# Kernel optimization log

Measured on AMD Instinct MI355X. Metric: run time of the kernel, lower is better.

## Reference

```python
import jax, jax.numpy as jnp
import numpy as np

N = 10000
F_IN = 512
HID = 256
C = 16
N_POST_ITER = 4


def setup_inputs() -> dict:
    key = jax.random.key(0)
    ks = jax.random.split(key, 10)
    raw_adj = jax.random.uniform(ks[0], (N, N), dtype=jnp.float32) * 0.01
    A = jax.random.uniform(ks[1], (N, N), dtype=jnp.float32)
    normed_adj = A / jnp.sum(A, axis=1, keepdims=True)  # row-sum-one normalized
    features = jax.random.normal(ks[2], (N, F_IN), dtype=jnp.float32)
    labels = jax.random.randint(ks[3], (N,), 0, C)
    y_onehot = jax.nn.one_hot(labels, C, dtype=jnp.float32)
    train_mask = jax.random.randint(ks[4], (N,), 0, 2).astype(jnp.bool_)
    # GCN belief estimator params (glorot-ish scaling)
    W1 = jax.random.normal(ks[5], (F_IN, HID), dtype=jnp.float32) / np.sqrt(F_IN)
    b1 = jnp.zeros((HID,), dtype=jnp.float32)
    W2 = jax.random.normal(ks[6], (HID, C), dtype=jnp.float32) / np.sqrt(HID)
    b2 = jnp.zeros((C,), dtype=jnp.float32)
    # class-compatibility matrix H (initialized, zero-centered as in init_H)
    H = jax.random.normal(ks[7], (C, C), dtype=jnp.float32) * 0.1
    return {"raw_adj": raw_adj, "normed_adj": normed_adj, "features": features,
            "y_onehot": y_onehot, "train_mask": train_mask,
            "W1": W1, "b1": b1, "W2": W2, "b2": b2, "H": H}


def reference(raw_adj, normed_adj, features, y_onehot, train_mask, W1, b1, W2, b2, H):
    num_class = y_onehot.shape[1]
    # 2-layer GCN belief estimator: adj @ (x @ W) + b
    h = jax.nn.relu(normed_adj @ (features @ W1) + b1)          # [N, HID]
    logits = normed_adj @ (h @ W2) + b2                          # [N, C]
    # post_process: iterative compatibility-guided belief propagation
    prior_belief = jax.nn.softmax(logits, axis=1)
    E_hat = prior_belief - 1.0 / num_class
    B_hat = E_hat
    for _ in range(N_POST_ITER):
        B_hat = E_hat + raw_adj @ (B_hat @ H)
    post_belief = B_hat + 1.0 / num_class
    return post_belief
```

## Files before the change

kernel.cpp:

```cpp
#include <hip/hip_runtime.h>

#define NN 10000
#define KP 10048
static constexpr float INV_C = 1.0f / 16.0f;

typedef __attribute__((ext_vector_type(8))) short bf16x8;
typedef __attribute__((ext_vector_type(4))) float f32x4;
typedef unsigned short u16;
typedef unsigned int u32;

__device__ __forceinline__ u16 f2b(float f) {
    union { float f; u32 u; } v; v.f = f;
    u32 r = v.u + 0x7FFFu + ((v.u >> 16) & 1u);
    return (u16)(r >> 16);
}

#define AS1(p) ((__attribute__((address_space(1))) void*)(p))
#define AS3(p) ((__attribute__((address_space(3))) void*)(p))

__global__ __launch_bounds__(256)
void cvt_feat(const float* __restrict__ src, u16* __restrict__ dst)
{
    int c = blockIdx.x * 256 + threadIdx.x;
    size_t base = (size_t)c * 8;
    const float4* s4 = (const float4*)(src + base);
    float4 a = s4[0], b = s4[1];
    bf16x8 o;
    o[0]=f2b(a.x); o[1]=f2b(a.y); o[2]=f2b(a.z); o[3]=f2b(a.w);
    o[4]=f2b(b.x); o[5]=f2b(b.y); o[6]=f2b(b.z); o[7]=f2b(b.w);
    *(bf16x8*)(dst + base) = o;
}

__global__ __launch_bounds__(256)
void w12t(const float* __restrict__ W1, const float* __restrict__ W2,
          float* __restrict__ W1T, u16* __restrict__ W2T)
{
    int bid = blockIdx.x, t = threadIdx.x;
    if (bid < 512) {
        int idx = bid * 256 + t;
        int n = idx >> 9, k = idx & 511;
        W1T[idx] = W1[(size_t)k * 256 + n];
    } else {
        int idx = (bid - 512) * 256 + t;
        if (idx < 4096) {
            int n_ = idx >> 8, k_ = idx & 255;
            W2T[idx] = f2b(W2[(size_t)k_ * 16 + n_]);
        }
    }
}

template<int BIAS, int RELU>
__global__ __launch_bounds__(256)
void gemm_a32_bt16(const float* __restrict__ A, int lda, int M, int Ka,
                   const u16* __restrict__ BT, int ldb, int N, int npad,
                   const float* __restrict__ bias,
                   u16* __restrict__ C, int ldc, int K)
{
    __shared__ u16 Asm[64 * 64];
    __shared__ u16 Bsm[256 * 64];
    const int t = threadIdx.x;
    const int lane = t & 63;
    const int w = t >> 6;
    const int row0 = blockIdx.x * 64;
    const int n0 = blockIdx.y * 256;

    const f32x4 fz = {0.f, 0.f, 0.f, 0.f};
    f32x4 acc[4][4];
#pragma unroll
    for (int i = 0; i < 4; ++i)
#pragma unroll
        for (int j = 0; j < 4; ++j) acc[i][j] = fz;

    const int ar = t >> 2, akq = t & 3;
    int agr = row0 + ar; if (agr > M - 1) agr = M - 1;
    const float* asrc = A + (size_t)agr * lda + akq * 16;
    const int aslot0 = (akq * 2) ^ (ar & 7);
    const int aslot1 = (akq * 2 + 1) ^ (ar & 7);
    const int l8 = lane >> 3, sl = lane & 7;

    for (int k0 = 0; k0 < K; k0 += 64) {
#pragma unroll
        for (int i = 0; i < 8; ++i) {
            int lr = i * 32 + w * 8 + l8;
            int gn = n0 + lr; if (gn > N - 1) gn = N - 1;
            int ss = sl ^ (lr & 7);
            const u16* src = BT + (size_t)gn * ldb + k0 + ss * 8;
            __builtin_amdgcn_global_load_lds(AS1(src), AS3(&Bsm[(i * 32 + w * 8) * 64]),
                                             16, 0, 0);
        }
        bool aval = (k0 + akq * 16) < Ka;
        float4 x0, x1, x2, x3;
        if (aval) {
            x0 = *(const float4*)(asrc + k0);
            x1 = *(const float4*)(asrc + k0 + 4);
            x2 = *(const float4*)(asrc + k0 + 8);
            x3 = *(const float4*)(asrc + k0 + 12);
        } else {
            x0 = x1 = x2 = x3 = make_float4(0.f, 0.f, 0.f, 0.f);
        }
        bf16x8 p0, p1;
        p0[0]=f2b(x0.x); p0[1]=f2b(x0.y); p0[2]=f2b(x0.z); p0[3]=f2b(x0.w);
        p0[4]=f2b(x1.x); p0[5]=f2b(x1.y); p0[6]=f2b(x1.z); p0[7]=f2b(x1.w);
        p1[0]=f2b(x2.x); p1[1]=f2b(x2.y); p1[2]=f2b(x2.z); p1[3]=f2b(x2.w);
        p1[4]=f2b(x3.x); p1[5]=f2b(x3.y); p1[6]=f2b(x3.z); p1[7]=f2b(x3.w);
        *(bf16x8*)&Asm[ar * 64 + aslot0 * 8] = p0;
        *(bf16x8*)&Asm[ar * 64 + aslot1 * 8] = p1;
        __syncthreads();
#pragma unroll
        for (int kk = 0; kk < 2; ++kk) {
            bf16x8 afr[4], bfr[4];
#pragma unroll
            for (int mi = 0; mi < 4; ++mi) {
                int r = mi * 16 + (lane & 15);
                int s2 = (kk * 4 + (lane >> 4)) ^ (r & 7);
                afr[mi] = *(const bf16x8*)&Asm[r * 64 + s2 * 8];
            }
#pragma unroll
            for (int ni = 0; ni < 4; ++ni) {
                int nr = w * 64 + ni * 16 + (lane & 15);
                int s2 = (kk * 4 + (lane >> 4)) ^ (nr & 7);
                bfr[ni] = *(const bf16x8*)&Bsm[nr * 64 + s2 * 8];
            }
#pragma unroll
            for (int mi = 0; mi < 4; ++mi)
#pragma unroll
                for (int ni = 0; ni < 4; ++ni)
                    acc[mi][ni] = __builtin_amdgcn_mfma_f32_16x16x32_bf16(
                        afr[mi], bfr[ni], acc[mi][ni], 0, 0, 0);
        }
        __syncthreads();
    }
#pragma unroll
    for (int mi = 0; mi < 4; ++mi) {
        int grb = row0 + mi * 16 + (lane >> 4) * 4;
#pragma unroll
        for (int ni = 0; ni < 4; ++ni) {
            int gc = n0 + w * 64 + ni * 16 + (lane & 15);
            if (gc < npad) {
                float bv = (BIAS && gc < N) ? bias[gc] : 0.f;
#pragma unroll
                for (int rg = 0; rg < 4; ++rg) {
                    int gr = grb + rg;
                    if (gr < M) {
                        float v = acc[mi][ni][rg] + bv;
                        if (RELU) v = fmaxf(v, 0.f);
                        C[(size_t)gr * ldc + gc] = f2b(gc < N ? v : 0.f);
                    }
                }
            }
        }
    }
}

template<int CVT>
__global__ __launch_bounds__(256)
void gemm_na(const float* __restrict__ A, const u16* __restrict__ BT,
             float* __restrict__ Pws, u16* __restrict__ Acvt)
{
    __shared__ u16 Asm[64 * 64];
    __shared__ u16 Bsm[256 * 64];
    const int t = threadIdx.x;
    const int lane = t & 63;
    const int w = t >> 6;
    const int row0 = blockIdx.x * 64;
    const int s = blockIdx.y;
    const int c0 = (157 * s) >> 3, c1 = (157 * (s + 1)) >> 3;

    const f32x4 fz = {0.f, 0.f, 0.f, 0.f};
    f32x4 acc[4][4];
#pragma unroll
    for (int i = 0; i < 4; ++i)
#pragma unroll
        for (int j = 0; j < 4; ++j) acc[i][j] = fz;

    const int ar = t >> 2, akq = t & 3;
    const int grow = row0 + ar;
    const int agr = grow < NN ? grow : NN - 1;
    const float* asrc = A + (size_t)agr * NN + akq * 16;
    const int aslot0 = (akq * 2) ^ (ar & 7);
    const int aslot1 = (akq * 2 + 1) ^ (ar & 7);
    const int l8 = lane >> 3, sl = lane & 7;

    for (int ck = c0; ck < c1; ++ck) {
        const int k0 = ck * 64;
#pragma unroll
        for (int i = 0; i < 8; ++i) {
            int lr = i * 32 + w * 8 + l8;
            int ss = sl ^ (lr & 7);
            const u16* src = BT + (size_t)lr * KP + k0 + ss * 8;
            __builtin_amdgcn_global_load_lds(AS1(src), AS3(&Bsm[(i * 32 + w * 8) * 64]),
                                             16, 0, 0);
        }
        const int kq0 = k0 + akq * 16;
        bool aval = kq0 < NN;
        float4 x0, x1, x2, x3;
        if (aval) {
            x0 = *(const float4*)(asrc + k0);
            x1 = *(const float4*)(asrc + k0 + 4);
            x2 = *(const float4*)(asrc + k0 + 8);
            x3 = *(const float4*)(asrc + k0 + 12);
        } else {
            x0 = x1 = x2 = x3 = make_float4(0.f, 0.f, 0.f, 0.f);
        }
        bf16x8 p0, p1;
        p0[0]=f2b(x0.x); p0[1]=f2b(x0.y); p0[2]=f2b(x0.z); p0[3]=f2b(x0.w);
        p0[4]=f2b(x1.x); p0[5]=f2b(x1.y); p0[6]=f2b(x1.z); p0[7]=f2b(x1.w);
        p1[0]=f2b(x2.x); p1[1]=f2b(x2.y); p1[2]=f2b(x2.z); p1[3]=f2b(x2.w);
        p1[4]=f2b(x3.x); p1[5]=f2b(x3.y); p1[6]=f2b(x3.z); p1[7]=f2b(x3.w);
        *(bf16x8*)&Asm[ar * 64 + aslot0 * 8] = p0;
        *(bf16x8*)&Asm[ar * 64 + aslot1 * 8] = p1;
        if (CVT && grow < NN) {
            *(bf16x8*)(Acvt + (size_t)grow * KP + kq0) = p0;
            *(bf16x8*)(Acvt + (size_t)grow * KP + kq0 + 8) = p1;
        }
        __syncthreads();
#pragma unroll
        for (int kk = 0; kk < 2; ++kk) {
            bf16x8 afr[4], bfr[4];
#pragma unroll
            for (int mi = 0; mi < 4; ++mi) {
                int r = mi * 16 + (lane & 15);
                int s2 = (kk * 4 + (lane >> 4)) ^ (r & 7);
                afr[mi] = *(const bf16x8*)&Asm[r * 64 + s2 * 8];
            }
#pragma unroll
            for (int ni = 0; ni < 4; ++ni) {
                int nr = w * 64 + ni * 16 + (lane & 15);
                int s2 = (kk * 4 + (lane >> 4)) ^ (nr & 7);
                bfr[ni] = *(const bf16x8*)&Bsm[nr * 64 + s2 * 8];
            }
#pragma unroll
            for (int mi = 0; mi < 4; ++mi)
#pragma unroll
                for (int ni = 0; ni < 4; ++ni)
                    acc[mi][ni] = __builtin_amdgcn_mfma_f32_16x16x32_bf16(
                        afr[mi], bfr[ni], acc[mi][ni], 0, 0, 0);
        }
        __syncthreads();
    }
    float* outp = Pws + (size_t)s * NN * 256;
#pragma unroll
    for (int mi = 0; mi < 4; ++mi) {
        int grb = row0 + mi * 16 + (lane >> 4) * 4;
#pragma unroll
        for (int ni = 0; ni < 4; ++ni) {
            int gc = w * 64 + ni * 16 + (lane & 15);
#pragma unroll
            for (int rg = 0; rg < 4; ++rg) {
                int gr = grb + rg;
                if (gr < NN)
                    outp[(size_t)gr * 256 + gc] = acc[mi][ni][rg];
            }
        }
    }
}

__global__ __launch_bounds__(256)
void reduce_h(const float* __restrict__ Pws, const float* __restrict__ b1,
              u16* __restrict__ hbf)
{
    int i8 = blockIdx.x * 256 + threadIdx.x;
    if (i8 >= NN * 256 / 8) return;
    size_t base = (size_t)i8 * 8;
    int col = (int)(base & 255);
    float v[8];
#pragma unroll
    for (int j = 0; j < 8; ++j) v[j] = b1[col + j];
#pragma unroll
    for (int s = 0; s < 8; ++s) {
        const float4* p = (const float4*)(Pws + (size_t)s * NN * 256 + base);
        float4 a = p[0], b = p[1];
        v[0]+=a.x; v[1]+=a.y; v[2]+=a.z; v[3]+=a.w;
        v[4]+=b.x; v[5]+=b.y; v[6]+=b.z; v[7]+=b.w;
    }
    bf16x8 o;
#pragma unroll
    for (int j = 0; j < 8; ++j) o[j] = f2b(fmaxf(v[j], 0.f));
    *(bf16x8*)(hbf + base) = o;
}

template<int AFP32, int CVT>
__global__ __launch_bounds__(256)
void adj16(const void* __restrict__ Av, long lda,
           const u16* __restrict__ BT,
           float* __restrict__ Pout, int nch, int nchf,
           u16* __restrict__ Acvt)
{
    const int t = threadIdx.x, lane = t & 63, w = t >> 6;
    const int s = blockIdx.y;
    const int rowu = blockIdx.x * 64 + w * 16 + (lane & 15);
    const int row = rowu < NN ? rowu : NN - 1;
    const int kq = (lane >> 4) * 8;
    const u16* brow = BT + (size_t)(lane & 15) * KP + kq;
    const float* a32 = (const float*)Av + (size_t)row * lda + kq;
    const u16*  a16 = (const u16*) Av + (size_t)row * lda + kq;
    u16* cvtp = CVT ? (Acvt + (size_t)rowu * KP + kq) : (u16*)0;
    const bool wok = CVT && (rowu < NN);

    int c0 = (nch * s) >> 3, c1 = (nch * (s + 1)) >> 3;
    int c1f = c1 < nchf ? c1 : nchf;
    f32x4 acc = {0.f, 0.f, 0.f, 0.f};
    int kc = c0;
    for (; kc + 4 <= c1f; kc += 4) {
        bf16x8 a[4], b[4];
#pragma unroll
        for (int u = 0; u < 4; ++u) {
            if (AFP32) {
                float4 x = *(const float4*)(a32 + (size_t)(kc + u) * 32);
                float4 y = *(const float4*)(a32 + (size_t)(kc + u) * 32 + 4);
                bf16x8 r;
                r[0]=f2b(x.x); r[1]=f2b(x.y); r[2]=f2b(x.z); r[3]=f2b(x.w);
                r[4]=f2b(y.x); r[5]=f2b(y.y); r[6]=f2b(y.z); r[7]=f2b(y.w);
                a[u] = r;
            } else {
                a[u] = *(const bf16x8*)(a16 + (size_t)(kc + u) * 32);
            }
            b[u] = *(const bf16x8*)(brow + (size_t)(kc + u) * 32);
        }
        if (CVT && wok) {
#pragma unroll
            for (int u = 0; u < 4; ++u)
                *(bf16x8*)(cvtp + (size_t)(kc + u) * 32) = a[u];
        }
#pragma unroll
        for (int u = 0; u < 4; ++u)
            acc = __builtin_amdgcn_mfma_f32_16x16x32_bf16(a[u], b[u], acc, 0, 0, 0);
    }
    for (; kc < c1; ++kc) {
        bf16x8 a = bf16x8{0,0,0,0,0,0,0,0};
        if (AFP32) {
            if (kc * 32 + kq < NN) {
                float4 x = *(const float4*)(a32 + (size_t)kc * 32);
                float4 y = *(const float4*)(a32 + (size_t)kc * 32 + 4);
                a[0]=f2b(x.x); a[1]=f2b(x.y); a[2]=f2b(x.z); a[3]=f2b(x.w);
                a[4]=f2b(y.x); a[5]=f2b(y.y); a[6]=f2b(y.z); a[7]=f2b(y.w);
            }
        } else {
            a = *(const bf16x8*)(a16 + (size_t)kc * 32);
        }
        if (CVT && wok)
            *(bf16x8*)(cvtp + (size_t)kc * 32) = a;
        bf16x8 b = *(const bf16x8*)(brow + (size_t)kc * 32);
        acc = __builtin_amdgcn_mfma_f32_16x16x32_bf16(a, b, acc, 0, 0, 0);
    }
    int ob = blockIdx.x * 64 + w * 16 + (lane >> 4) * 4;
#pragma unroll
    for (int rg = 0; rg < 4; ++rg) {
        int orow = ob + rg;
        if (orow < NN)
            Pout[(size_t)s * (NN * 16) + (size_t)orow * 16 + (lane & 15)] = acc[rg];
    }
}

__global__ __launch_bounds__(256)
void hw2_mfma(const u16* __restrict__ h, const u16* __restrict__ W2T,
              u16* __restrict__ outT)
{
    const int t = threadIdx.x, lane = t & 63, w = t >> 6;
    int row = blockIdx.x * 64 + w * 16 + (lane & 15);
    int rowc = row < NN ? row : NN - 1;
    const int kq = (lane >> 4) * 8;
    const u16* arow = h + (size_t)rowc * 256 + kq;
    const u16* brow = W2T + (size_t)(lane & 15) * 256 + kq;
    f32x4 acc = {0.f, 0.f, 0.f, 0.f};
#pragma unroll
    for (int kc = 0; kc < 8; ++kc) {
        bf16x8 a = *(const bf16x8*)(arow + kc * 32);
        bf16x8 b = *(const bf16x8*)(brow + kc * 32);
        acc = __builtin_amdgcn_mfma_f32_16x16x32_bf16(a, b, acc, 0, 0, 0);
    }
    int ob = blockIdx.x * 64 + w * 16 + (lane >> 4) * 4;
    int col = lane & 15;
#pragma unroll
    for (int rg = 0; rg < 4; ++rg) {
        int r = ob + rg;
        outT[(size_t)col * KP + r] = f2b(r < NN ? acc[rg] : 0.f);
    }
}

__global__ __launch_bounds__(256)
void softmax_e_h(const float* __restrict__ P, const float* __restrict__ b2,
                 const float* __restrict__ H, float* __restrict__ E,
                 u16* __restrict__ bhT)
{
    __shared__ float Hs[256];
    const int t = threadIdx.x;
    Hs[t] = H[t];
    __syncthreads();
    int r = blockIdx.x * 256 + t;
    if (r >= KP) return;
    float l[16];
    if (r < NN) {
#pragma unroll
        for (int k = 0; k < 16; ++k) l[k] = b2[k];
#pragma unroll
        for (int s = 0; s < 8; ++s) {
            const float4* p4 = (const float4*)(P + (size_t)s * (NN * 16) + (size_t)r * 16);
            float4 a = p4[0], b = p4[1], c = p4[2], d = p4[3];
            l[0]+=a.x;  l[1]+=a.y;  l[2]+=a.z;  l[3]+=a.w;
            l[4]+=b.x;  l[5]+=b.y;  l[6]+=b.z;  l[7]+=b.w;
            l[8]+=c.x;  l[9]+=c.y;  l[10]+=c.z; l[11]+=c.w;
            l[12]+=d.x; l[13]+=d.y; l[14]+=d.z; l[15]+=d.w;
        }
        float mx = l[0];
#pragma unroll
        for (int k = 1; k < 16; ++k) mx = fmaxf(mx, l[k]);
        float ssum = 0.f;
#pragma unroll
        for (int k = 0; k < 16; ++k) { l[k] = __expf(l[k] - mx); ssum += l[k]; }
        float inv = 1.f / ssum;
#pragma unroll
        for (int k = 0; k < 16; ++k) {
            l[k] = l[k] * inv - INV_C;
            E[(size_t)r * 16 + k] = l[k];
        }
    } else {
#pragma unroll
        for (int k = 0; k < 16; ++k) l[k] = 0.f;
    }
    float acc[16];
#pragma unroll
    for (int k = 0; k < 16; ++k) acc[k] = 0.f;
#pragma unroll
    for (int m = 0; m < 16; ++m) {
        float x = l[m];
        const float4* h4 = (const float4*)&Hs[m * 16];
#pragma unroll
        for (int k4 = 0; k4 < 4; ++k4) {
            float4 hh = h4[k4];
            acc[k4*4+0] += x * hh.x; acc[k4*4+1] += x * hh.y;
            acc[k4*4+2] += x * hh.z; acc[k4*4+3] += x * hh.w;
        }
    }
#pragma unroll
    for (int k = 0; k < 16; ++k)
        bhT[(size_t)k * KP + r] = f2b(acc[k]);
}

template<int LAST>
__global__ __launch_bounds__(256)
void combine_bmm(const float* __restrict__ E, const float* __restrict__ P,
                 const float* __restrict__ H, u16* __restrict__ bhT,
                 float* __restrict__ out)
{
    __shared__ float Hs[256];
    const int t = threadIdx.x;
    Hs[t] = H[t];
    __syncthreads();
    int r = blockIdx.x * 256 + t;
    if (r >= KP) return;
    float Bv[16];
    if (r < NN) {
        const float4* e4 = (const float4*)(E + (size_t)r * 16);
        float4 a = e4[0], b = e4[1], c = e4[2], d = e4[3];
        Bv[0]=a.x;  Bv[1]=a.y;  Bv[2]=a.z;  Bv[3]=a.w;
        Bv[4]=b.x;  Bv[5]=b.y;  Bv[6]=b.z;  Bv[7]=b.w;
        Bv[8]=c.x;  Bv[9]=c.y;  Bv[10]=c.z; Bv[11]=c.w;
        Bv[12]=d.x; Bv[13]=d.y; Bv[14]=d.z; Bv[15]=d.w;
#pragma unroll
        for (int s = 0; s < 8; ++s) {
            const float4* p4 = (const float4*)(P + (size_t)s * (NN * 16) + (size_t)r * 16);
            float4 pa = p4[0], pb = p4[1], pc = p4[2], pd = p4[3];
            Bv[0]+=pa.x;  Bv[1]+=pa.y;  Bv[2]+=pa.z;  Bv[3]+=pa.w;
            Bv[4]+=pb.x;  Bv[5]+=pb.y;  Bv[6]+=pb.z;  Bv[7]+=pb.w;
            Bv[8]+=pc.x;  Bv[9]+=pc.y;  Bv[10]+=pc.z; Bv[11]+=pc.w;
            Bv[12]+=pd.x; Bv[13]+=pd.y; Bv[14]+=pd.z; Bv[15]+=pd.w;
        }
    } else {
#pragma unroll
        for (int k = 0; k < 16; ++k) Bv[k] = 0.f;
    }
    if (LAST) {
        if (r < NN) {
            float4 o[4];
#pragma unroll
            for (int q = 0; q < 4; ++q) {
                o[q].x = Bv[q*4+0] + INV_C; o[q].y = Bv[q*4+1] + INV_C;
                o[q].z = Bv[q*4+2] + INV_C; o[q].w = Bv[q*4+3] + INV_C;
                ((float4*)(out + (size_t)r * 16))[q] = o[q];
            }
        }
    } else {
        float acc[16];
#pragma unroll
        for (int k = 0; k < 16; ++k) acc[k] = 0.f;
#pragma unroll
        for (int m = 0; m < 16; ++m) {
            float x = Bv[m];
            const float4* h4 = (const float4*)&Hs[m * 16];
#pragma unroll
            for (int k4 = 0; k4 < 4; ++k4) {
                float4 hh = h4[k4];
                acc[k4*4+0] += x * hh.x; acc[k4*4+1] += x * hh.y;
                acc[k4*4+2] += x * hh.z; acc[k4*4+3] += x * hh.w;
            }
        }
#pragma unroll
        for (int k = 0; k < 16; ++k)
            bhT[(size_t)k * KP + r] = f2b(acc[k]);
    }
}

extern "C" void kernel_launch(void* const* d_in, const int* in_sizes, int n_in,
                              void* d_out, int out_size, void* d_ws, size_t ws_size,
                              hipStream_t stream)
{
    const float* raw_adj    = (const float*)d_in[0];
    const float* normed_adj = (const float*)d_in[1];
    const float* features   = (const float*)d_in[2];
    const float* W1 = (const float*)d_in[5];
    const float* b1 = (const float*)d_in[6];
    const float* W2 = (const float*)d_in[7];
    const float* b2 = (const float*)d_in[8];
    const float* H  = (const float*)d_in[9];
    float* out = (float*)d_out;

    char* ws = (char*)d_ws;
    u16*   featbf = (u16*)  (ws + 0);
    float* P      = (float*)(ws + 0);
    float* E      = (float*)(ws + 5120000);
    float* W1T    = (float*)(ws + 10240000);
    u16*   W2T    = (u16*)  (ws + 10764288);
    u16*   XWT    = (u16*)  (ws + 10772480);
    u16*   hbf    = (u16*)  (ws + 15917056);
    u16*   hw2T   = (u16*)  (ws + 21037056);
    u16*   bhT    = (u16*)  (ws + 21358592);
    const bool full  = ws_size >= (size_t)304560128;
    const bool mid   = ws_size >= (size_t)222640128;
    const bool low   = ws_size >= (size_t)103600128;
    u16*   An_bf = (u16*)  (ws + 21680128);
    float* Pws   = (float*)(ws + (full ? 222640128 : 21680128));
    u16*   ArBf  = (u16*)  (ws + 21680128);

    cvt_feat<<<2500, 256, 0, stream>>>(features, featbf);
    w12t<<<528, 256, 0, stream>>>(W1, W2, W1T, W2T);

    gemm_a32_bt16<0, 0><<<dim3(4, 40), 256, 0, stream>>>(
        W1T, 512, 256, 512, featbf, 512, NN, KP, nullptr, XWT, KP, 512);

    if (low) {
        if (full)
            gemm_na<1><<<dim3(157, 8), 256, 0, stream>>>(normed_adj, XWT, Pws, An_bf);
        else
            gemm_na<0><<<dim3(157, 8), 256, 0, stream>>>(normed_adj, XWT, Pws, nullptr);
        reduce_h<<<1250, 256, 0, stream>>>(Pws, b1, hbf);
    } else {
        gemm_a32_bt16<1, 1><<<dim3(157, 1), 256, 0, stream>>>(
            normed_adj, NN, NN, NN, XWT, KP, 256, 256, b1, hbf, 256, KP);
    }

    hw2_mfma<<<157, 256, 0, stream>>>(hbf, W2T, hw2T);

    if (full)
        adj16<0, 0><<<dim3(157, 8), 256, 0, stream>>>(
            (const void*)An_bf, KP, hw2T, P, 314, 314, nullptr);
    else
        adj16<1, 0><<<dim3(157, 8), 256, 0, stream>>>(
            (const void*)normed_adj, NN, hw2T, P, 313, 312, nullptr);

    softmax_e_h<<<40, 256, 0, stream>>>(P, b2, H, E, bhT);

    for (int it = 0; it < 4; ++it) {
        if (mid) {
            if (it == 0)
                adj16<1, 1><<<dim3(157, 8), 256, 0, stream>>>(
                    (const void*)raw_adj, NN, bhT, P, 314, 312, ArBf);
            else
                adj16<0, 0><<<dim3(157, 8), 256, 0, stream>>>(
                    (const void*)ArBf, KP, bhT, P, 314, 314, nullptr);
        } else {
            adj16<1, 0><<<dim3(157, 8), 256, 0, stream>>>(
                (const void*)raw_adj, NN, bhT, P, 313, 312, nullptr);
        }
        if (it == 3)
            combine_bmm<1><<<40, 256, 0, stream>>>(E, P, H, nullptr, out);
        else
            combine_bmm<0><<<40, 256, 0, stream>>>(E, P, H, bhT, nullptr);
    }
}
```

Before: 609.1 us.

## Use nontemporal loads, bf16 split-K partials, and 4-thread-per-row epilogue kernels

Streaming fp32 adjacency and feature reads now use nontemporal loads, and the converted bf16 adjacency read in the first layer-2 pass is loaded nontemporally too. The split-K partials of the first GCN layer are stored as bf16 instead of fp32, which halves workspace traffic and lowers the workspace threshold for the fast paths, at the cost of extra rounding error. The softmax and combine epilogues now give each row to four threads with shuffle reductions and launch 157 blocks instead of 40, to raise parallelism in these small kernels.

```diff
diff --git a/kernel.cpp b/kernel.cpp
--- a/kernel.cpp
+++ b/kernel.cpp
@@ -14,20 +14,26 @@
     u32 r = v.u + 0x7FFFu + ((v.u >> 16) & 1u);
     return (u16)(r >> 16);
 }
+__device__ __forceinline__ float b2f(u16 b) {
+    union { u32 u; float f; } v; v.u = ((u32)b) << 16;
+    return v.f;
+}
 
 #define AS1(p) ((__attribute__((address_space(1))) void*)(p))
 #define AS3(p) ((__attribute__((address_space(3))) void*)(p))
+#define NTL4(p)  __builtin_nontemporal_load((const f32x4*)(p))
+#define NTL8H(p) __builtin_nontemporal_load((const bf16x8*)(p))
 
 __global__ __launch_bounds__(256)
 void cvt_feat(const float* __restrict__ src, u16* __restrict__ dst)
 {
     int c = blockIdx.x * 256 + threadIdx.x;
     size_t base = (size_t)c * 8;
-    const float4* s4 = (const float4*)(src + base);
-    float4 a = s4[0], b = s4[1];
+    f32x4 a = NTL4(src + base);
+    f32x4 b = NTL4(src + base + 4);
     bf16x8 o;
-    o[0]=f2b(a.x); o[1]=f2b(a.y); o[2]=f2b(a.z); o[3]=f2b(a.w);
-    o[4]=f2b(b.x); o[5]=f2b(b.y); o[6]=f2b(b.z); o[7]=f2b(b.w);
+    o[0]=f2b(a[0]); o[1]=f2b(a[1]); o[2]=f2b(a[2]); o[3]=f2b(a[3]);
+    o[4]=f2b(b[0]); o[5]=f2b(b[1]); o[6]=f2b(b[2]); o[7]=f2b(b[3]);
     *(bf16x8*)(dst + base) = o;
 }
 
@@ -89,20 +95,20 @@
                                              16, 0, 0);
         }
         bool aval = (k0 + akq * 16) < Ka;
-        float4 x0, x1, x2, x3;
+        f32x4 x0, x1, x2, x3;
         if (aval) {
-            x0 = *(const float4*)(asrc + k0);
-            x1 = *(const float4*)(asrc + k0 + 4);
-            x2 = *(const float4*)(asrc + k0 + 8);
-            x3 = *(const float4*)(asrc + k0 + 12);
+            x0 = *(const f32x4*)(asrc + k0);
+            x1 = *(const f32x4*)(asrc + k0 + 4);
+            x2 = *(const f32x4*)(asrc + k0 + 8);
+            x3 = *(const f32x4*)(asrc + k0 + 12);
         } else {
-            x0 = x1 = x2 = x3 = make_float4(0.f, 0.f, 0.f, 0.f);
+            x0 = x1 = x2 = x3 = fz;
         }
         bf16x8 p0, p1;
-        p0[0]=f2b(x0.x); p0[1]=f2b(x0.y); p0[2]=f2b(x0.z); p0[3]=f2b(x0.w);
-        p0[4]=f2b(x1.x); p0[5]=f2b(x1.y); p0[6]=f2b(x1.z); p0[7]=f2b(x1.w);
-        p1[0]=f2b(x2.x); p1[1]=f2b(x2.y); p1[2]=f2b(x2.z); p1[3]=f2b(x2.w);
-        p1[4]=f2b(x3.x); p1[5]=f2b(x3.y); p1[6]=f2b(x3.z); p1[7]=f2b(x3.w);
+        p0[0]=f2b(x0[0]); p0[1]=f2b(x0[1]); p0[2]=f2b(x0[2]); p0[3]=f2b(x0[3]);
+        p0[4]=f2b(x1[0]); p0[5]=f2b(x1[1]); p0[6]=f2b(x1[2]); p0[7]=f2b(x1[3]);
+        p1[0]=f2b(x2[0]); p1[1]=f2b(x2[1]); p1[2]=f2b(x2[2]); p1[3]=f2b(x2[3]);
+        p1[4]=f2b(x3[0]); p1[5]=f2b(x3[1]); p1[6]=f2b(x3[2]); p1[7]=f2b(x3[3]);
         *(bf16x8*)&Asm[ar * 64 + aslot0 * 8] = p0;
         *(bf16x8*)&Asm[ar * 64 + aslot1 * 8] = p1;
         __syncthreads();
@@ -155,7 +161,7 @@
 template<int CVT>
 __global__ __launch_bounds__(256)
 void gemm_na(const float* __restrict__ A, const u16* __restrict__ BT,
-             float* __restrict__ Pws, u16* __restrict__ Acvt)
+             u16* __restrict__ Pws, u16* __restrict__ Acvt)
 {
     __shared__ u16 Asm[64 * 64];
     __shared__ u16 Bsm[256 * 64];
@@ -193,20 +199,20 @@
         }
         const int kq0 = k0 + akq * 16;
         bool aval = kq0 < NN;
-        float4 x0, x1, x2, x3;
+        f32x4 x0, x1, x2, x3;
         if (aval) {
-            x0 = *(const float4*)(asrc + k0);
-            x1 = *(const float4*)(asrc + k0 + 4);
-            x2 = *(const float4*)(asrc + k0 + 8);
-            x3 = *(const float4*)(asrc + k0 + 12);
+            x0 = NTL4(asrc + k0);
+            x1 = NTL4(asrc + k0 + 4);
+            x2 = NTL4(asrc + k0 + 8);
+            x3 = NTL4(asrc + k0 + 12);
         } else {
-            x0 = x1 = x2 = x3 = make_float4(0.f, 0.f, 0.f, 0.f);
+            x0 = x1 = x2 = x3 = fz;
         }
         bf16x8 p0, p1;
-        p0[0]=f2b(x0.x); p0[1]=f2b(x0.y); p0[2]=f2b(x0.z); p0[3]=f2b(x0.w);
-        p0[4]=f2b(x1.x); p0[5]=f2b(x1.y); p0[6]=f2b(x1.z); p0[7]=f2b(x1.w);
-        p1[0]=f2b(x2.x); p1[1]=f2b(x2.y); p1[2]=f2b(x2.z); p1[3]=f2b(x2.w);
-        p1[4]=f2b(x3.x); p1[5]=f2b(x3.y); p1[6]=f2b(x3.z); p1[7]=f2b(x3.w);
+        p0[0]=f2b(x0[0]); p0[1]=f2b(x0[1]); p0[2]=f2b(x0[2]); p0[3]=f2b(x0[3]);
+        p0[4]=f2b(x1[0]); p0[5]=f2b(x1[1]); p0[6]=f2b(x1[2]); p0[7]=f2b(x1[3]);
+        p1[0]=f2b(x2[0]); p1[1]=f2b(x2[1]); p1[2]=f2b(x2[2]); p1[3]=f2b(x2[3]);
+        p1[4]=f2b(x3[0]); p1[5]=f2b(x3[1]); p1[6]=f2b(x3[2]); p1[7]=f2b(x3[3]);
         *(bf16x8*)&Asm[ar * 64 + aslot0 * 8] = p0;
         *(bf16x8*)&Asm[ar * 64 + aslot1 * 8] = p1;
         if (CVT && grow < NN) {
@@ -238,7 +244,7 @@
         }
         __syncthreads();
     }
-    float* outp = Pws + (size_t)s * NN * 256;
+    u16* outp = Pws + (size_t)s * NN * 256;
 #pragma unroll
     for (int mi = 0; mi < 4; ++mi) {
         int grb = row0 + mi * 16 + (lane >> 4) * 4;
@@ -249,18 +255,17 @@
             for (int rg = 0; rg < 4; ++rg) {
                 int gr = grb + rg;
                 if (gr < NN)
-                    outp[(size_t)gr * 256 + gc] = acc[mi][ni][rg];
-            }
-        }
-    }
-}
-
-__global__ __launch_bounds__(256)
-void reduce_h(const float* __restrict__ Pws, const float* __restrict__ b1,
+                    outp[(size_t)gr * 256 + gc] = f2b(acc[mi][ni][rg]);
+            }
+        }
+    }
+}
+
+__global__ __launch_bounds__(256)
+void reduce_h(const u16* __restrict__ Pws, const float* __restrict__ b1,
               u16* __restrict__ hbf)
 {
     int i8 = blockIdx.x * 256 + threadIdx.x;
-    if (i8 >= NN * 256 / 8) return;
     size_t base = (size_t)i8 * 8;
     int col = (int)(base & 255);
     float v[8];
@@ -268,10 +273,9 @@
     for (int j = 0; j < 8; ++j) v[j] = b1[col + j];
 #pragma unroll
     for (int s = 0; s < 8; ++s) {
-        const float4* p = (const float4*)(Pws + (size_t)s * NN * 256 + base);
-        float4 a = p[0], b = p[1];
-        v[0]+=a.x; v[1]+=a.y; v[2]+=a.z; v[3]+=a.w;
-        v[4]+=b.x; v[5]+=b.y; v[6]+=b.z; v[7]+=b.w;
+        bf16x8 p = NTL8H(Pws + (size_t)s * NN * 256 + base);
+#pragma unroll
+        for (int j = 0; j < 8; ++j) v[j] += b2f((u16)p[j]);
     }
     bf16x8 o;
 #pragma unroll
@@ -279,7 +283,7 @@
     *(bf16x8*)(hbf + base) = o;
 }
 
-template<int AFP32, int CVT>
+template<int AFP32, int CVT, int NTA16>
 __global__ __launch_bounds__(256)
 void adj16(const void* __restrict__ Av, long lda,
            const u16* __restrict__ BT,
@@ -306,12 +310,14 @@
 #pragma unroll
         for (int u = 0; u < 4; ++u) {
             if (AFP32) {
-                float4 x = *(const float4*)(a32 + (size_t)(kc + u) * 32);
-                float4 y = *(const float4*)(a32 + (size_t)(kc + u) * 32 + 4);
+                f32x4 x = NTL4(a32 + (size_t)(kc + u) * 32);
+                f32x4 y = NTL4(a32 + (size_t)(kc + u) * 32 + 4);
                 bf16x8 r;
-                r[0]=f2b(x.x); r[1]=f2b(x.y); r[2]=f2b(x.z); r[3]=f2b(x.w);
-                r[4]=f2b(y.x); r[5]=f2b(y.y); r[6]=f2b(y.z); r[7]=f2b(y.w);
+                r[0]=f2b(x[0]); r[1]=f2b(x[1]); r[2]=f2b(x[2]); r[3]=f2b(x[3]);
+                r[4]=f2b(y[0]); r[5]=f2b(y[1]); r[6]=f2b(y[2]); r[7]=f2b(y[3]);
                 a[u] = r;
+            } else if (NTA16) {
+                a[u] = NTL8H(a16 + (size_t)(kc + u) * 32);
             } else {
                 a[u] = *(const bf16x8*)(a16 + (size_t)(kc + u) * 32);
             }
@@ -330,10 +336,10 @@
         bf16x8 a = bf16x8{0,0,0,0,0,0,0,0};
         if (AFP32) {
             if (kc * 32 + kq < NN) {
-                float4 x = *(const float4*)(a32 + (size_t)kc * 32);
-                float4 y = *(const float4*)(a32 + (size_t)kc * 32 + 4);
-                a[0]=f2b(x.x); a[1]=f2b(x.y); a[2]=f2b(x.z); a[3]=f2b(x.w);
-                a[4]=f2b(y.x); a[5]=f2b(y.y); a[6]=f2b(y.z); a[7]=f2b(y.w);
+                f32x4 x = NTL4(a32 + (size_t)kc * 32);
+                f32x4 y = NTL4(a32 + (size_t)kc * 32 + 4);
+                a[0]=f2b(x[0]); a[1]=f2b(x[1]); a[2]=f2b(x[2]); a[3]=f2b(x[3]);
+                a[4]=f2b(y[0]); a[5]=f2b(y[1]); a[6]=f2b(y[2]); a[7]=f2b(y[3]);
             }
         } else {
             a = *(const bf16x8*)(a16 + (size_t)kc * 32);
@@ -379,125 +385,127 @@
 }
 
 __global__ __launch_bounds__(256)
-void softmax_e_h(const float* __restrict__ P, const float* __restrict__ b2,
-                 const float* __restrict__ H, float* __restrict__ E,
-                 u16* __restrict__ bhT)
+void softmax_e_h2(const float* __restrict__ P, const float* __restrict__ b2,
+                  const float* __restrict__ H, float* __restrict__ E,
+                  u16* __restrict__ bhT)
 {
     __shared__ float Hs[256];
     const int t = threadIdx.x;
     Hs[t] = H[t];
     __syncthreads();
-    int r = blockIdx.x * 256 + t;
-    if (r >= KP) return;
-    float l[16];
-    if (r < NN) {
-#pragma unroll
-        for (int k = 0; k < 16; ++k) l[k] = b2[k];
-#pragma unroll
-        for (int s = 0; s < 8; ++s) {
-            const float4* p4 = (const float4*)(P + (size_t)s * (NN * 16) + (size_t)r * 16);
-            float4 a = p4[0], b = p4[1], c = p4[2], d = p4[3];
-            l[0]+=a.x;  l[1]+=a.y;  l[2]+=a.z;  l[3]+=a.w;
-            l[4]+=b.x;  l[5]+=b.y;  l[6]+=b.z;  l[7]+=b.w;
-            l[8]+=c.x;  l[9]+=c.y;  l[10]+=c.z; l[11]+=c.w;
-            l[12]+=d.x; l[13]+=d.y; l[14]+=d.z; l[15]+=d.w;
-        }
-        float mx = l[0];
-#pragma unroll
-        for (int k = 1; k < 16; ++k) mx = fmaxf(mx, l[k]);
+    const int l = t & 63, w = t >> 6;
+    const int g = l >> 2, sub = l & 3;
+    const int row = blockIdx.x * 64 + w * 16 + g;
+    const bool valid = row < NN;
+    float acc[16];
+#pragma unroll
+    for (int k = 0; k < 16; ++k) acc[k] = 0.f;
+    if (valid) {
+        const float* p0 = P + (size_t)(sub * 2) * (NN * 16) + (size_t)row * 16;
+        const float* p1 = p0 + (size_t)NN * 16;
+#pragma unroll
+        for (int q = 0; q < 4; ++q) {
+            f32x4 a = *(const f32x4*)(p0 + q * 4);
+            f32x4 c = *(const f32x4*)(p1 + q * 4);
+#pragma unroll
+            for (int j = 0; j < 4; ++j) acc[q * 4 + j] = a[j] + c[j];
+        }
+        if (sub == 0) {
+#pragma unroll
+            for (int k = 0; k < 16; ++k) acc[k] += b2[k];
+        }
+    }
+#pragma unroll
+    for (int m = 1; m <= 2; m <<= 1)
+#pragma unroll
+        for (int k = 0; k < 16; ++k) acc[k] += __shfl_xor(acc[k], m, 4);
+    float e[16];
+    if (valid) {
+        float mx = acc[0];
+#pragma unroll
+        for (int k = 1; k < 16; ++k) mx = fmaxf(mx, acc[k]);
         float ssum = 0.f;
 #pragma unroll
-        for (int k = 0; k < 16; ++k) { l[k] = __expf(l[k] - mx); ssum += l[k]; }
+        for (int k = 0; k < 16; ++k) { e[k] = __expf(acc[k] - mx); ssum += e[k]; }
         float inv = 1.f / ssum;
 #pragma unroll
-        for (int k = 0; k < 16; ++k) {
-            l[k] = l[k] * inv - INV_C;
-            E[(size_t)r * 16 + k] = l[k];
-        }
+        for (int k = 0; k < 16; ++k) e[k] = e[k] * inv - INV_C;
+        f32x4 eq = {e[sub*4+0], e[sub*4+1], e[sub*4+2], e[sub*4+3]};
+        *(f32x4*)(E + (size_t)row * 16 + sub * 4) = eq;
     } else {
 #pragma unroll
-        for (int k = 0; k < 16; ++k) l[k] = 0.f;
-    }
-    float acc[16];
-#pragma unroll
-    for (int k = 0; k < 16; ++k) acc[k] = 0.f;
-#pragma unroll
-    for (int m = 0; m < 16; ++m) {
-        float x = l[m];
-        const float4* h4 = (const float4*)&Hs[m * 16];
-#pragma unroll
-        for (int k4 = 0; k4 < 4; ++k4) {
-            float4 hh = h4[k4];
-            acc[k4*4+0] += x * hh.x; acc[k4*4+1] += x * hh.y;
-            acc[k4*4+2] += x * hh.z; acc[k4*4+3] += x * hh.w;
-        }
-    }
-#pragma unroll
-    for (int k = 0; k < 16; ++k)
-        bhT[(size_t)k * KP + r] = f2b(acc[k]);
+        for (int k = 0; k < 16; ++k) e[k] = 0.f;
+    }
+    float o[4] = {0.f, 0.f, 0.f, 0.f};
+#pragma unroll
+    for (int m2 = 0; m2 < 16; ++m2) {
+        float x = e[m2];
+#pragma unroll
+        for (int j = 0; j < 4; ++j) o[j] += x * Hs[m2 * 16 + sub * 4 + j];
+    }
+#pragma unroll
+    for (int j = 0; j < 4; ++j)
+        bhT[(size_t)(sub * 4 + j) * KP + row] = f2b(o[j]);
 }
 
 template<int LAST>
 __global__ __launch_bounds__(256)
-void combine_bmm(const float* __restrict__ E, const float* __restrict__ P,
-                 const float* __restrict__ H, u16* __restrict__ bhT,
-                 float* __restrict__ out)
+void combine_bmm2(const float* __restrict__ E, const float* __restrict__ P,
+                  const float* __restrict__ H, u16* __restrict__ bhT,
+                  float* __restrict__ out)
 {
     __shared__ float Hs[256];
     const int t = threadIdx.x;
     Hs[t] = H[t];
     __syncthreads();
-    int r = blockIdx.x * 256 + t;
-    if (r >= KP) return;
-    float Bv[16];
-    if (r < NN) {
-        const float4* e4 = (const float4*)(E + (size_t)r * 16);
-        float4 a = e4[0], b = e4[1], c = e4[2], d = e4[3];
-        Bv[0]=a.x;  Bv[1]=a.y;  Bv[2]=a.z;  Bv[3]=a.w;
-        Bv[4]=b.x;  Bv[5]=b.y;  Bv[6]=b.z;  Bv[7]=b.w;
-        Bv[8]=c.x;  Bv[9]=c.y;  Bv[10]=c.z; Bv[11]=c.w;
-        Bv[12]=d.x; Bv[13]=d.y; Bv[14]=d.z; Bv[15]=d.w;
-#pragma unroll
-        for (int s = 0; s < 8; ++s) {
-            const float4* p4 = (const float4*)(P + (size_t)s * (NN * 16) + (size_t)r * 16);
-            float4 pa = p4[0], pb = p4[1], pc = p4[2], pd = p4[3];
-            Bv[0]+=pa.x;  Bv[1]+=pa.y;  Bv[2]+=pa.z;  Bv[3]+=pa.w;
-            Bv[4]+=pb.x;  Bv[5]+=pb.y;  Bv[6]+=pb.z;  Bv[7]+=pb.w;
-            Bv[8]+=pc.x;  Bv[9]+=pc.y;  Bv[10]+=pc.z; Bv[11]+=pc.w;
-            Bv[12]+=pd.x; Bv[13]+=pd.y; Bv[14]+=pd.z; Bv[15]+=pd.w;
+    const int l = t & 63, w = t >> 6;
+    const int g = l >> 2, sub = l & 3;
+    const int row = blockIdx.x * 64 + w * 16 + g;
+    const bool valid = row < NN;
+    float acc[16];
+#pragma unroll
+    for (int k = 0; k < 16; ++k) acc[k] = 0.f;
+    if (valid) {
+        const float* p0 = P + (size_t)(sub * 2) * (NN * 16) + (size_t)row * 16;
+        const float* p1 = p0 + (size_t)NN * 16;
+#pragma unroll
+        for (int q = 0; q < 4; ++q) {
+            f32x4 a = *(const f32x4*)(p0 + q * 4);
+            f32x4 c = *(const f32x4*)(p1 + q * 4);
+#pragma unroll
+            for (int j = 0; j < 4; ++j) acc[q * 4 + j] = a[j] + c[j];
+        }
+        if (sub == 0) {
+            const float* ep = E + (size_t)row * 16;
+#pragma unroll
+            for (int k = 0; k < 16; ++k) acc[k] += ep[k];
+        }
+    }
+#pragma unroll
+    for (int m = 1; m <= 2; m <<= 1)
+#pragma unroll
+        for (int k = 0; k < 16; ++k) acc[k] += __shfl_xor(acc[k], m, 4);
+    if (LAST) {
+        if (valid) {
+            f32x4 oq = {acc[sub*4+0] + INV_C, acc[sub*4+1] + INV_C,
+                        acc[sub*4+2] + INV_C, acc[sub*4+3] + INV_C};
+            *(f32x4*)(out + (size_t)row * 16 + sub * 4) = oq;
         }
     } else {
-#pragma unroll
-        for (int k = 0; k < 16; ++k) Bv[k] = 0.f;
-    }
-    if (LAST) {
-        if (r < NN) {
-            float4 o[4];
-#pragma unroll
-            for (int q = 0; q < 4; ++q) {
-                o[q].x = Bv[q*4+0] + INV_C; o[q].y = Bv[q*4+1] + INV_C;
-                o[q].z = Bv[q*4+2] + INV_C; o[q].w = Bv[q*4+3] + INV_C;
-                ((float4*)(out + (size_t)r * 16))[q] = o[q];
-            }
-        }
-    } else {
-        float acc[16];
-#pragma unroll
-        for (int k = 0; k < 16; ++k) acc[k] = 0.f;
-#pragma unroll
-        for (int m = 0; m < 16; ++m) {
-            float x = Bv[m];
-            const float4* h4 = (const float4*)&Hs[m * 16];
-#pragma unroll
-            for (int k4 = 0; k4 < 4; ++k4) {
-                float4 hh = h4[k4];
-                acc[k4*4+0] += x * hh.x; acc[k4*4+1] += x * hh.y;
-                acc[k4*4+2] += x * hh.z; acc[k4*4+3] += x * hh.w;
-            }
-        }
-#pragma unroll
-        for (int k = 0; k < 16; ++k)
-            bhT[(size_t)k * KP + r] = f2b(acc[k]);
+        if (!valid) {
+#pragma unroll
+            for (int k = 0; k < 16; ++k) acc[k] = 0.f;
+        }
+        float o[4] = {0.f, 0.f, 0.f, 0.f};
+#pragma unroll
+        for (int m2 = 0; m2 < 16; ++m2) {
+            float x = acc[m2];
+#pragma unroll
+            for (int j = 0; j < 4; ++j) o[j] += x * Hs[m2 * 16 + sub * 4 + j];
+        }
+#pragma unroll
+        for (int j = 0; j < 4; ++j)
+            bhT[(size_t)(sub * 4 + j) * KP + row] = f2b(o[j]);
     }
 }
 
@@ -525,12 +533,12 @@
     u16*   hbf    = (u16*)  (ws + 15917056);
     u16*   hw2T   = (u16*)  (ws + 21037056);
     u16*   bhT    = (u16*)  (ws + 21358592);
-    const bool full  = ws_size >= (size_t)304560128;
-    const bool mid   = ws_size >= (size_t)222640128;
-    const bool low   = ws_size >= (size_t)103600128;
-    u16*   An_bf = (u16*)  (ws + 21680128);
-    float* Pws   = (float*)(ws + (full ? 222640128 : 21680128));
-    u16*   ArBf  = (u16*)  (ws + 21680128);
+    const bool full = ws_size >= (size_t)263600128;
+    const bool mid  = ws_size >= (size_t)222640128;
+    const bool low  = ws_size >= (size_t)62640128;
+    u16* An_bf = (u16*)(ws + 21680128);
+    u16* ArBf  = (u16*)(ws + 21680128);
+    u16* Pws   = (u16*)(ws + (full ? 222640128 : 21680128));
 
     cvt_feat<<<2500, 256, 0, stream>>>(features, featbf);
     w12t<<<528, 256, 0, stream>>>(W1, W2, W1T, W2T);
@@ -552,29 +560,29 @@
     hw2_mfma<<<157, 256, 0, stream>>>(hbf, W2T, hw2T);
 
     if (full)
-        adj16<0, 0><<<dim3(157, 8), 256, 0, stream>>>(
+        adj16<0, 0, 1><<<dim3(157, 8), 256, 0, stream>>>(
             (const void*)An_bf, KP, hw2T, P, 314, 314, nullptr);
     else
-        adj16<1, 0><<<dim3(157, 8), 256, 0, stream>>>(
+        adj16<1, 0, 0><<<dim3(157, 8), 256, 0, stream>>>(
             (const void*)normed_adj, NN, hw2T, P, 313, 312, nullptr);
 
-    softmax_e_h<<<40, 256, 0, stream>>>(P, b2, H, E, bhT);
+    softmax_e_h2<<<157, 256, 0, stream>>>(P, b2, H, E, bhT);
 
     for (int it = 0; it < 4; ++it) {
         if (mid) {
             if (it == 0)
-                adj16<1, 1><<<dim3(157, 8), 256, 0, stream>>>(
+                adj16<1, 1, 0><<<dim3(157, 8), 256, 0, stream>>>(
                     (const void*)raw_adj, NN, bhT, P, 314, 312, ArBf);
             else
-                adj16<0, 0><<<dim3(157, 8), 256, 0, stream>>>(
+                adj16<0, 0, 0><<<dim3(157, 8), 256, 0, stream>>>(
                     (const void*)ArBf, KP, bhT, P, 314, 314, nullptr);
         } else {
-            adj16<1, 0><<<dim3(157, 8), 256, 0, stream>>>(
+            adj16<1, 0, 0><<<dim3(157, 8), 256, 0, stream>>>(
                 (const void*)raw_adj, NN, bhT, P, 313, 312, nullptr);
         }
         if (it == 3)
-            combine_bmm<1><<<40, 256, 0, stream>>>(E, P, H, nullptr, out);
+            combine_bmm2<1><<<157, 256, 0, stream>>>(E, P, H, nullptr, out);
         else
-            combine_bmm<0><<<40, 256, 0, stream>>>(E, P, H, bhT, nullptr);
-    }
-}
+            combine_bmm2<0><<<157, 256, 0, stream>>>(E, P, H, bhT, nullptr);
+    }
+}
```

New measurement: 670.0 us. +10.0%, slower.
